# Kernel tuning notes

Hardware: AMD Instinct MI355X
Metric: run time of the kernel (lower is better)

Reference implementation:

```python
import jax, jax.numpy as jnp
import numpy as np

GAMMA = 1.0

C, K, D = 10000, 4, 2048  # classes, prototypes per class, feature dim


def setup_inputs() -> dict:
    key = jax.random.key(0)
    k1, k2 = jax.random.split(key)
    feature = jax.random.normal(k1, (D,), dtype=jnp.float32)
    all_prototypes = jax.random.normal(k2, (C, K, D), dtype=jnp.float32)
    label = 7
    return {"feature": feature, "label": label, "all_prototypes": all_prototypes}


def reference(feature, label, all_prototypes):
    # squared euclidean distance from feature to every prototype: [C, K]
    diff = all_prototypes - feature  # broadcast [C,K,D]
    d = jnp.sum(diff * diff, axis=-1)  # [C,K]
    logits = -GAMMA * d  # [C,K]
    # denominator: one = sum_{c,k} exp(-gamma * d_{c,k}); use stable logsumexp
    log_one = jax.nn.logsumexp(logits)
    # probability = sum_k -log(exp(logits[label,k]) / one)
    #             = sum_k (gamma * d[label,k] + log(one))
    lbl_logits = jax.lax.dynamic_index_in_dim(logits, label, axis=0, keepdims=False)  # [K]
    probability = jnp.sum(log_one - lbl_logits)
    return probability
```

## Files before the change

### kernel.cpp

```cpp
#include <hip/hip_runtime.h>

#define C_CLASSES 10000
#define K_PROTO   4
#define D_DIM     2048
#define ROWS      (C_CLASSES * K_PROTO)
#define D_VEC     (D_DIM / 4)
#define RPW       5
#define NBLOCKS   2000
#define NWAVES    (NBLOCKS * 4)

__global__ __launch_bounds__(256) void dist_kernel(const float4* __restrict__ proto,
                                                   const float4* __restrict__ feat,
                                                   const int* __restrict__ label,
                                                   float* __restrict__ wave_min,
                                                   float* __restrict__ wave_sum,
                                                   float* __restrict__ d_label) {
    const int wave = (blockIdx.x << 2) | (threadIdx.x >> 6);
    const int lane = threadIdx.x & 63;
    const int row0 = wave * RPW;
    const int lbl  = label[0];

    float4 f[8];
#pragma unroll
    for (int j = 0; j < 8; ++j) f[j] = feat[j * 64 + lane];

    float d[RPW];
#pragma unroll
    for (int r = 0; r < RPW; ++r) {
        const float4* p = proto + (size_t)(row0 + r) * D_VEC;
        float acc = 0.0f;
#pragma unroll
        for (int j = 0; j < 8; ++j) {
            const float4 pv = p[j * 64 + lane];
            const float dx = pv.x - f[j].x;
            const float dy = pv.y - f[j].y;
            const float dz = pv.z - f[j].z;
            const float dw = pv.w - f[j].w;
            acc += dx * dx + dy * dy + dz * dz + dw * dw;
        }
#pragma unroll
        for (int mask = 1; mask < 64; mask <<= 1)
            acc += __shfl_xor(acc, mask, 64);
        d[r] = acc;
    }

    float mw = d[0];
#pragma unroll
    for (int r = 1; r < RPW; ++r) mw = fminf(mw, d[r]);
    float sw = 0.0f;
#pragma unroll
    for (int r = 0; r < RPW; ++r) sw += expf(mw - d[r]);

    if (lane == 0) {
        wave_min[wave] = mw;
        wave_sum[wave] = sw;
#pragma unroll
        for (int r = 0; r < RPW; ++r) {
            const int row = row0 + r;
            if ((row >> 2) == lbl) d_label[row & 3] = d[r];
        }
    }
}

__global__ __launch_bounds__(256) void finalize_kernel(const float* __restrict__ wave_min,
                                                       const float* __restrict__ wave_sum,
                                                       const float* __restrict__ d_label,
                                                       float* __restrict__ out) {
    __shared__ float red[256];
    const int tid = threadIdx.x;

    float m = 3.402823466e38f;
    for (int i = tid; i < NWAVES; i += 256) m = fminf(m, wave_min[i]);
    red[tid] = m;
    __syncthreads();
    for (int s = 128; s > 0; s >>= 1) {
        if (tid < s) red[tid] = fminf(red[tid], red[tid + s]);
        __syncthreads();
    }
    const float dmin = red[0];
    __syncthreads();

    float acc = 0.0f;
    for (int i = tid; i < NWAVES; i += 256)
        acc += wave_sum[i] * expf(dmin - wave_min[i]);
    red[tid] = acc;
    __syncthreads();
    for (int s = 128; s > 0; s >>= 1) {
        if (tid < s) red[tid] += red[tid + s];
        __syncthreads();
    }

    if (tid == 0) {
        const float log_one = -dmin + logf(red[0]);
        float p = 0.0f;
#pragma unroll
        for (int k = 0; k < K_PROTO; ++k) p += log_one + d_label[k];
        out[0] = p;
    }
}

extern "C" void kernel_launch(void* const* d_in, const int* in_sizes, int n_in,
                              void* d_out, int out_size, void* d_ws, size_t ws_size,
                              hipStream_t stream) {
    const float* feat  = (const float*)d_in[0];
    const int*   label = (const int*)d_in[1];
    const float* proto = (const float*)d_in[2];
    float* out = (float*)d_out;

    float* wave_min = (float*)d_ws;
    float* wave_sum = wave_min + NWAVES;
    float* d_label  = wave_sum + NWAVES;

    dist_kernel<<<NBLOCKS, 256, 0, stream>>>(
        (const float4*)proto, (const float4*)feat, label,
        wave_min, wave_sum, d_label);
    finalize_kernel<<<1, 256, 0, stream>>>(wave_min, wave_sum, d_label, out);
}
```

Before: 460.0 us.

## Give each wave one class with double-buffered prototype loads and merged reductions

Each wave now handles exactly four rows (one class) instead of five, with more blocks launched. Prototype rows are loaded into two alternating register buffers so the next row's loads are issued while the current row is computed. The four per-row cross-lane reductions are merged into one transposed butterfly, and the per-wave min and sum are packed into a float2. The intent is more memory-level parallelism and fewer shuffles on a bandwidth-bound scan, at the cost of higher register pressure from the double buffers.

```diff
diff --git a/kernel.cpp b/kernel.cpp
--- a/kernel.cpp
+++ b/kernel.cpp
@@ -5,72 +5,93 @@
 #define D_DIM     2048
 #define ROWS      (C_CLASSES * K_PROTO)
 #define D_VEC     (D_DIM / 4)
-#define RPW       5
-#define NBLOCKS   2000
+#define RPW       4
+#define NBLOCKS   2500
 #define NWAVES    (NBLOCKS * 4)
 
 __global__ __launch_bounds__(256) void dist_kernel(const float4* __restrict__ proto,
                                                    const float4* __restrict__ feat,
                                                    const int* __restrict__ label,
-                                                   float* __restrict__ wave_min,
-                                                   float* __restrict__ wave_sum,
+                                                   float2* __restrict__ wave_pair,
                                                    float* __restrict__ d_label) {
     const int wave = (blockIdx.x << 2) | (threadIdx.x >> 6);
     const int lane = threadIdx.x & 63;
-    const int row0 = wave * RPW;
     const int lbl  = label[0];
+    const float4* p0 = proto + (size_t)wave * RPW * D_VEC;
 
     float4 f[8];
 #pragma unroll
     for (int j = 0; j < 8; ++j) f[j] = feat[j * 64 + lane];
 
-    float d[RPW];
+    float4 a[8], b[8];
 #pragma unroll
-    for (int r = 0; r < RPW; ++r) {
-        const float4* p = proto + (size_t)(row0 + r) * D_VEC;
-        float acc = 0.0f;
+    for (int j = 0; j < 8; ++j) a[j] = p0[j * 64 + lane];
 #pragma unroll
-        for (int j = 0; j < 8; ++j) {
-            const float4 pv = p[j * 64 + lane];
-            const float dx = pv.x - f[j].x;
-            const float dy = pv.y - f[j].y;
-            const float dz = pv.z - f[j].z;
-            const float dw = pv.w - f[j].w;
-            acc += dx * dx + dy * dy + dz * dz + dw * dw;
-        }
+    for (int j = 0; j < 8; ++j) b[j] = p0[D_VEC + j * 64 + lane];
+
+    float acc0 = 0.f, acc1 = 0.f, acc2 = 0.f, acc3 = 0.f;
 #pragma unroll
-        for (int mask = 1; mask < 64; mask <<= 1)
-            acc += __shfl_xor(acc, mask, 64);
-        d[r] = acc;
+    for (int j = 0; j < 8; ++j) {
+        const float dx = a[j].x - f[j].x, dy = a[j].y - f[j].y;
+        const float dz = a[j].z - f[j].z, dw = a[j].w - f[j].w;
+        acc0 += dx * dx + dy * dy + dz * dz + dw * dw;
+    }
+#pragma unroll
+    for (int j = 0; j < 8; ++j) a[j] = p0[2 * D_VEC + j * 64 + lane];
+#pragma unroll
+    for (int j = 0; j < 8; ++j) {
+        const float dx = b[j].x - f[j].x, dy = b[j].y - f[j].y;
+        const float dz = b[j].z - f[j].z, dw = b[j].w - f[j].w;
+        acc1 += dx * dx + dy * dy + dz * dz + dw * dw;
+    }
+#pragma unroll
+    for (int j = 0; j < 8; ++j) b[j] = p0[3 * D_VEC + j * 64 + lane];
+#pragma unroll
+    for (int j = 0; j < 8; ++j) {
+        const float dx = a[j].x - f[j].x, dy = a[j].y - f[j].y;
+        const float dz = a[j].z - f[j].z, dw = a[j].w - f[j].w;
+        acc2 += dx * dx + dy * dy + dz * dz + dw * dw;
+    }
+#pragma unroll
+    for (int j = 0; j < 8; ++j) {
+        const float dx = b[j].x - f[j].x, dy = b[j].y - f[j].y;
+        const float dz = b[j].z - f[j].z, dw = b[j].w - f[j].w;
+        acc3 += dx * dx + dy * dy + dz * dz + dw * dw;
     }
 
-    float mw = d[0];
 #pragma unroll
-    for (int r = 1; r < RPW; ++r) mw = fminf(mw, d[r]);
-    float sw = 0.0f;
+    for (int m = 1; m <= 2; m <<= 1) {
+        acc0 += __shfl_xor(acc0, m, 64);
+        acc1 += __shfl_xor(acc1, m, 64);
+        acc2 += __shfl_xor(acc2, m, 64);
+        acc3 += __shfl_xor(acc3, m, 64);
+    }
+    const int l3 = lane & 3;
+    float v = acc0;
+    v = (l3 == 1) ? acc1 : v;
+    v = (l3 == 2) ? acc2 : v;
+    v = (l3 == 3) ? acc3 : v;
 #pragma unroll
-    for (int r = 0; r < RPW; ++r) sw += expf(mw - d[r]);
+    for (int m = 4; m <= 32; m <<= 1) v += __shfl_xor(v, m, 64);
 
-    if (lane == 0) {
-        wave_min[wave] = mw;
-        wave_sum[wave] = sw;
-#pragma unroll
-        for (int r = 0; r < RPW; ++r) {
-            const int row = row0 + r;
-            if ((row >> 2) == lbl) d_label[row & 3] = d[r];
-        }
-    }
+    float mn = fminf(v, __shfl_xor(v, 1, 64));
+    mn = fminf(mn, __shfl_xor(mn, 2, 64));
+    float s = expf(mn - v);
+    s += __shfl_xor(s, 1, 64);
+    s += __shfl_xor(s, 2, 64);
+
+    if (lane == 0) wave_pair[wave] = make_float2(mn, s);
+    if (wave == lbl && lane < 4) d_label[lane] = v;
 }
 
-__global__ __launch_bounds__(256) void finalize_kernel(const float* __restrict__ wave_min,
-                                                       const float* __restrict__ wave_sum,
+__global__ __launch_bounds__(256) void finalize_kernel(const float2* __restrict__ wave_pair,
                                                        const float* __restrict__ d_label,
                                                        float* __restrict__ out) {
     __shared__ float red[256];
     const int tid = threadIdx.x;
 
     float m = 3.402823466e38f;
-    for (int i = tid; i < NWAVES; i += 256) m = fminf(m, wave_min[i]);
+    for (int i = tid; i < NWAVES; i += 256) m = fminf(m, wave_pair[i].x);
     red[tid] = m;
     __syncthreads();
     for (int s = 128; s > 0; s >>= 1) {
@@ -81,8 +102,10 @@
     __syncthreads();
 
     float acc = 0.0f;
-    for (int i = tid; i < NWAVES; i += 256)
-        acc += wave_sum[i] * expf(dmin - wave_min[i]);
+    for (int i = tid; i < NWAVES; i += 256) {
+        const float2 p = wave_pair[i];
+        acc += p.y * expf(dmin - p.x);
+    }
     red[tid] = acc;
     __syncthreads();
     for (int s = 128; s > 0; s >>= 1) {
@@ -107,12 +130,10 @@
     const float* proto = (const float*)d_in[2];
     float* out = (float*)d_out;
 
-    float* wave_min = (float*)d_ws;
-    float* wave_sum = wave_min + NWAVES;
-    float* d_label  = wave_sum + NWAVES;
+    float2* wave_pair = (float2*)d_ws;
+    float*  d_label   = (float*)(wave_pair + NWAVES);
 
     dist_kernel<<<NBLOCKS, 256, 0, stream>>>(
-        (const float4*)proto, (const float4*)feat, label,
-        wave_min, wave_sum, d_label);
-    finalize_kernel<<<1, 256, 0, stream>>>(wave_min, wave_sum, d_label, out);
+        (const float4*)proto, (const float4*)feat, label, wave_pair, d_label);
+    finalize_kernel<<<1, 256, 0, stream>>>(wave_pair, d_label, out);
 }
```

Measured after the change: 435.9 us. 1.06x faster.
